# Kernel tuning notes

Hardware: AMD Instinct MI355X
Metric: run time of the kernel (lower is better)

## Reference

```python
import jax, jax.numpy as jnp
import numpy as np

DIM = 1536
NH = 12
HD = DIM // NH  # 128
B = 1
F, H, W = 8, 16, 16
S = F * H * W  # 2048
EPS = 1e-6
MAX_POS = 1024


def _rmsnorm(x, g):
    # WanRMSNorm: x * rsqrt(mean(x^2, -1) + eps) * weight  (computed in fp32)
    return x * jax.lax.rsqrt(jnp.mean(x * x, axis=-1, keepdims=True) + EPS) * g


def _rope_apply(x, grid_sizes, freqs):
    # x: [B, S, NH, HD]; freqs: [1024, HD//2] angles. Full (level-0) freqs_i path.
    f, h, w = [int(v) for v in np.asarray(grid_sizes[0])]
    c = HD // 2  # 64
    s0 = c - 2 * (c // 3)  # 22 (frame freqs)
    s1 = c // 3            # 21 (height / width freqs)
    p0 = freqs[:f, :s0]
    p1 = freqs[:h, s0:s0 + s1]
    p2 = freqs[:w, s0 + s1:]
    ang = jnp.concatenate([
        jnp.broadcast_to(p0[:, None, None, :], (f, h, w, s0)),
        jnp.broadcast_to(p1[None, :, None, :], (f, h, w, s1)),
        jnp.broadcast_to(p2[None, None, :, :], (f, h, w, s1)),
    ], axis=-1).reshape(f * h * w, 1, c)  # [S, 1, c]
    cos, sin = jnp.cos(ang), jnp.sin(ang)
    xr = x[0].reshape(S, NH, c, 2)  # pairs -> complex rotation
    x0, x1 = xr[..., 0], xr[..., 1]
    out = jnp.stack([x0 * cos - x1 * sin, x0 * sin + x1 * cos], axis=-1)
    return out.reshape(S, NH, HD)[None].astype(jnp.float32)  # [1, S, NH, HD]


def setup_inputs() -> dict:
    key = jax.random.key(0)
    ks = jax.random.split(key, 8)
    sc = 0.02
    return {
        "x": jax.random.normal(ks[0], (B, S, DIM), jnp.float32),
        "freqs": jax.random.uniform(ks[1], (MAX_POS, HD // 2), jnp.float32, 0.0, 2.0 * np.pi),
        "wq": jax.random.normal(ks[2], (DIM, DIM), jnp.float32) * sc,
        "bq": jnp.zeros((DIM,), jnp.float32),
        "wk": jax.random.normal(ks[3], (DIM, DIM), jnp.float32) * sc,
        "bk": jnp.zeros((DIM,), jnp.float32),
        "wv": jax.random.normal(ks[4], (DIM, DIM), jnp.float32) * sc,
        "bv": jnp.zeros((DIM,), jnp.float32),
        "wo": jax.random.normal(ks[5], (DIM, DIM), jnp.float32) * sc,
        "bo": jnp.zeros((DIM,), jnp.float32),
        "gq": jnp.ones((DIM,), jnp.float32),
        "gk": jnp.ones((DIM,), jnp.float32),
        "seq_lens": jnp.array([S], jnp.int32),
        "grid_sizes": jnp.array([[F, H, W]], jnp.int32),
    }


def reference(x, freqs, wq, bq, wk, bk, wv, bv, wo, bo, gq, gk, seq_lens, grid_sizes):
    b, s = x.shape[:2]
    q = _rmsnorm(x @ wq.T + bq, gq).reshape(b, s, NH, HD)
    k = _rmsnorm(x @ wk.T + bk, gk).reshape(b, s, NH, HD)
    v = (x @ wv.T + bv).reshape(b, s, NH, HD)
    q = _rope_apply(q, grid_sizes, freqs)
    k = _rope_apply(k, grid_sizes, freqs)
    # flash_attention with k_lens=seq_lens, full window -> masked SDPA
    kmask = jnp.arange(s)[None, :] < seq_lens[:, None]  # [b, s]
    scores = jnp.einsum('bqnd,bknd->bnqk', q, k) / np.sqrt(HD).astype(np.float32)
    scores = jnp.where(kmask[:, None, None, :], scores, jnp.finfo(scores.dtype).min)
    attn = jax.nn.softmax(scores, axis=-1)
    out = jnp.einsum('bnqk,bknd->bqnd', attn, v).reshape(b, s, DIM)
    return out @ wo.T + bo
```

## Files before the change

kernel.cpp:

```cpp
#include <hip/hip_runtime.h>
#include <math.h>

#define DIMN 1536
#define NHEAD 12
#define HDIM 128
#define SLEN 2048
#define EPSV 1e-6f

typedef __attribute__((ext_vector_type(8))) short short8;
typedef __attribute__((ext_vector_type(4))) short short4v;
typedef __attribute__((ext_vector_type(4))) float f32x4;

typedef __attribute__((address_space(1))) const void gvoid_t;
typedef __attribute__((address_space(3))) void lvoid_t;

__device__ __forceinline__ void gload_lds16(const void* g, void* l) {
    __builtin_amdgcn_global_load_lds((gvoid_t*)g, (lvoid_t*)l, 16, 0, 0);
}

__device__ inline short to_bf16(float f) {
    union { float f; unsigned u; } v; v.f = f;
    unsigned r = (v.u + 0x7FFFu + ((v.u >> 16) & 1u)) >> 16;
    return (short)r;
}
__device__ inline float bf_to_f(short h) {
    union { unsigned u; float f; } v;
    v.u = ((unsigned)(unsigned short)h) << 16;
    return v.f;
}

__device__ __forceinline__ int swz8(int row, int c) {
    return c ^ (row & 7);
}

__global__ __launch_bounds__(256)
void cast5(const float* s0, const float* s1, const float* s2,
           const float* s3, const float* s4,
           short* d0, short* d1, short* d2, short* d3, short* d4,
           int n0, int nw)
{
    const float* s; short* d; int n;
    switch (blockIdx.y) {
        case 0: s = s0; d = d0; n = n0; break;
        case 1: s = s1; d = d1; n = nw; break;
        case 2: s = s2; d = d2; n = nw; break;
        case 3: s = s3; d = d3; n = nw; break;
        default: s = s4; d = d4; n = nw; break;
    }
    int idx = (blockIdx.x * 256 + threadIdx.x) * 8;
    if (idx >= n) return;
    float4 a = *(const float4*)(s + idx);
    float4 b = *(const float4*)(s + idx + 4);
    short8 r;
    r[0] = to_bf16(a.x); r[1] = to_bf16(a.y); r[2] = to_bf16(a.z); r[3] = to_bf16(a.w);
    r[4] = to_bf16(b.x); r[5] = to_bf16(b.y); r[6] = to_bf16(b.z); r[7] = to_bf16(b.w);
    *(short8*)(d + idx) = r;
}

__device__ __forceinline__ void gemm_mainloop(const short* __restrict__ A,
    const short* __restrict__ W, int m0, int n0, int K,
    short* As, short* Bs, f32x4 (&acc)[4][4])
{
    const int tid = threadIdx.x;
    const int wave = tid >> 6, lane = tid & 63;
    const int quad = lane >> 4, col = lane & 15;
    const int wm = wave >> 1, wn = wave & 1;
    const int sr = tid >> 3;
    const int sc = tid & 7;

    for (int kt = 0; kt < K; kt += 64) {
        __syncthreads();
        #pragma unroll
        for (int i = 0; i < 4; ++i) {
            const int row = i * 32 + sr;
            const int c = swz8(row, sc);
            gload_lds16(A + (size_t)(m0 + row) * K + kt + c * 8, As + i * 2048 + tid * 8);
        }
        #pragma unroll
        for (int i = 0; i < 4; ++i) {
            const int row = i * 32 + sr;
            const int c = swz8(row, sc);
            gload_lds16(W + (size_t)(n0 + row) * K + kt + c * 8, Bs + i * 2048 + tid * 8);
        }
        __syncthreads();

        #pragma unroll
        for (int kb = 0; kb < 2; ++kb) {
            short8 af[4], bf[4];
            #pragma unroll
            for (int mt = 0; mt < 4; ++mt) {
                const int row = wm * 64 + mt * 16 + col;
                af[mt] = *(const short8*)&As[row * 64 + swz8(row, kb * 4 + quad) * 8];
            }
            #pragma unroll
            for (int nt = 0; nt < 4; ++nt) {
                const int row = wn * 64 + nt * 16 + col;
                bf[nt] = *(const short8*)&Bs[row * 64 + swz8(row, kb * 4 + quad) * 8];
            }
            #pragma unroll
            for (int mt = 0; mt < 4; ++mt)
                #pragma unroll
                for (int nt = 0; nt < 4; ++nt)
                    acc[mt][nt] = __builtin_amdgcn_mfma_f32_16x16x32_bf16(
                        af[mt], bf[nt], acc[mt][nt], 0, 0, 0);
        }
    }
}

__global__ __launch_bounds__(256)
void gemm_qkv(const short* __restrict__ A,
              const short* __restrict__ W0, const short* __restrict__ W1,
              const short* __restrict__ W2,
              const float* __restrict__ b0, const float* __restrict__ b1,
              const float* __restrict__ b2,
              short* __restrict__ Y0, short* __restrict__ Y1,
              short* __restrict__ Vp)
{
    __shared__ __attribute__((aligned(16))) short As[128 * 64];
    __shared__ __attribute__((aligned(16))) short Bs[128 * 64];

    const int sel = blockIdx.x / (DIMN / 128);
    const int nb  = blockIdx.x % (DIMN / 128);
    const short* W    = (sel == 0) ? W0 : (sel == 1) ? W1 : W2;
    const float* bias = (sel == 0) ? b0 : (sel == 1) ? b1 : b2;

    const int tid = threadIdx.x;
    const int wave = tid >> 6, lane = tid & 63;
    const int quad = lane >> 4, col = lane & 15;
    const int wm = wave >> 1, wn = wave & 1;
    const int m0 = blockIdx.y * 128, n0 = nb * 128;

    f32x4 acc[4][4];
    #pragma unroll
    for (int i = 0; i < 4; ++i)
        #pragma unroll
        for (int j = 0; j < 4; ++j)
            #pragma unroll
            for (int r = 0; r < 4; ++r) acc[i][j][r] = 0.f;

    gemm_mainloop(A, W, m0, n0, DIMN, As, Bs, acc);

    if (sel < 2) {
        short* Y = (sel == 0) ? Y0 : Y1;
        #pragma unroll
        for (int mt = 0; mt < 4; ++mt) {
            #pragma unroll
            for (int nt = 0; nt < 4; ++nt) {
                const int n = n0 + wn * 64 + nt * 16 + col;
                const float bb = bias[n];
                #pragma unroll
                for (int r = 0; r < 4; ++r) {
                    const int m = m0 + wm * 64 + mt * 16 + quad * 4 + r;
                    Y[(size_t)m * DIMN + n] = to_bf16(acc[mt][nt][r] + bb);
                }
            }
        }
    } else {
        const int head = nb;
        const int kt64 = blockIdx.y * 2 + wm;
        #pragma unroll
        for (int mt = 0; mt < 4; ++mt) {
            #pragma unroll
            for (int nt = 0; nt < 4; ++nt) {
                const int n = n0 + wn * 64 + nt * 16 + col;
                const float bb = bias[n];
                const int dt = wn * 4 + nt;
                const int chunk = (head * 64 + kt64 * 2 + (mt >> 1)) * 8 + dt;
                const int off = ((mt & 1) * 2 + (quad >> 1)) * 128 + col * 8 + (quad & 1) * 4;
                short4v o;
                #pragma unroll
                for (int r = 0; r < 4; ++r) o[r] = to_bf16(acc[mt][nt][r] + bb);
                *(short4v*)(Vp + (size_t)chunk * 512 + off) = o;
            }
        }
    }
}

__global__ __launch_bounds__(256)
void gemm_out(const short* __restrict__ A, const short* __restrict__ W,
              const float* __restrict__ bias, float* __restrict__ Yf)
{
    __shared__ __attribute__((aligned(16))) short As[128 * 64];
    __shared__ __attribute__((aligned(16))) short Bs[128 * 64];

    const int tid = threadIdx.x;
    const int wave = tid >> 6, lane = tid & 63;
    const int quad = lane >> 4, col = lane & 15;
    const int wm = wave >> 1, wn = wave & 1;
    const int m0 = blockIdx.y * 128, n0 = blockIdx.x * 128;

    f32x4 acc[4][4];
    #pragma unroll
    for (int i = 0; i < 4; ++i)
        #pragma unroll
        for (int j = 0; j < 4; ++j)
            #pragma unroll
            for (int r = 0; r < 4; ++r) acc[i][j][r] = 0.f;

    gemm_mainloop(A, W, m0, n0, DIMN, As, Bs, acc);

    #pragma unroll
    for (int mt = 0; mt < 4; ++mt) {
        #pragma unroll
        for (int nt = 0; nt < 4; ++nt) {
            const int n = n0 + wn * 64 + nt * 16 + col;
            const float bb = bias[n];
            #pragma unroll
            for (int r = 0; r < 4; ++r) {
                const int m = m0 + wm * 64 + mt * 16 + quad * 4 + r;
                Yf[(size_t)m * DIMN + n] = acc[mt][nt][r] + bb;
            }
        }
    }
}

__global__ __launch_bounds__(256)
void rms_rope_qk(short* __restrict__ qbuf, const short* __restrict__ kbuf,
                 short* __restrict__ Kp,
                 const float* __restrict__ gq, const float* __restrict__ gk,
                 const float* __restrict__ freqs, const int* __restrict__ grid_sizes)
{
    const int s = blockIdx.x;
    const int isK = blockIdx.y;
    const int tid = threadIdx.x;
    short* qrow = qbuf + (size_t)s * DIMN;
    const short* row = isK ? (kbuf + (size_t)s * DIMN) : qrow;
    const float* g = isK ? gk : gq;

    float ss = 0.f;
    if (tid < 192) {
        short8 v = *(const short8*)(row + tid * 8);
        #pragma unroll
        for (int j = 0; j < 8; ++j) { float f = bf_to_f(v[j]); ss += f * f; }
    }
    #pragma unroll
    for (int off = 32; off; off >>= 1) ss += __shfl_down(ss, off, 64);

    __shared__ float red[4];
    __shared__ float s_scale;
    if ((tid & 63) == 0) red[tid >> 6] = ss;
    __syncthreads();
    if (tid == 0) {
        float t = red[0] + red[1] + red[2] + red[3];
        float sc = rsqrtf(t / (float)DIMN + EPSV);
        s_scale = isK ? sc : sc * 0.08838834764831845f;
    }
    __syncthreads();
    const float scale = s_scale;

    const int h = grid_sizes[1], w = grid_sizes[2];
    const int fi = s / (h * w);
    const int hi = (s / w) % h;
    const int wi = s % w;

    if (!isK) {
        for (int p = tid; p < NHEAD * 64; p += 256) {
            const int n = p >> 6;
            const int d = p & 63;
            const int idx = (d < 22) ? fi : ((d < 43) ? hi : wi);
            const float ang = freqs[idx * 64 + d];
            float sn, cs;
            __sincosf(ang, &sn, &cs);
            const int base = n * HDIM + 2 * d;
            const float v0 = bf_to_f(qrow[base]) * scale * g[base];
            const float v1 = bf_to_f(qrow[base + 1]) * scale * g[base + 1];
            qrow[base]     = to_bf16(v0 * cs - v1 * sn);
            qrow[base + 1] = to_bf16(v0 * sn + v1 * cs);
        }
    } else if (tid < 192) {
        const int n = tid >> 4;
        const int o = tid & 15;
        short8 outv;
        #pragma unroll
        for (int pp = 0; pp < 4; ++pp) {
            const int pd = o * 4 + pp;
            const int idx = (pd < 22) ? fi : ((pd < 43) ? hi : wi);
            const float ang = freqs[idx * 64 + pd];
            float sn, cs;
            __sincosf(ang, &sn, &cs);
            const int base = n * HDIM + 2 * pd;
            const float v0 = bf_to_f(row[base]) * scale * g[base];
            const float v1 = bf_to_f(row[base + 1]) * scale * g[base + 1];
            outv[pp * 2]     = to_bf16(v0 * cs - v1 * sn);
            outv[pp * 2 + 1] = to_bf16(v0 * sn + v1 * cs);
        }
        const int kb = s >> 4, colk = s & 15;
        const int kc = o >> 2, quadk = o & 3;
        const size_t addr = ((((size_t)(n * 128 + kb) * 4 + kc) * 64) + quadk * 16 + colk) * 8;
        *(short8*)(Kp + addr) = outv;
    }
}

__global__ __launch_bounds__(128)
void attn_mfma11(const short* __restrict__ Q, const short* __restrict__ Kp,
                 const short* __restrict__ Vp, short* __restrict__ O,
                 const int* __restrict__ seq_lens)
{
    __shared__ __attribute__((aligned(16))) short psw[2 * 1280];
    __shared__ __attribute__((aligned(16))) float sacc[32 * 132];
    __shared__ float sl[32];

    const int tid  = threadIdx.x;
    const int wave = tid >> 6;
    const int lane = tid & 63;
    const int quad = lane >> 4, col = lane & 15;

    const int orig = blockIdx.y * 64 + blockIdx.x;
    const int work = (orig & 7) * 96 + (orig >> 3);
    const int head = work >> 6;
    const int row0 = (work & 63) * 32;
    const int slen = seq_lens[0];

    short8 qf[2][4];
    #pragma unroll
    for (int T = 0; T < 2; ++T)
        #pragma unroll
        for (int kc = 0; kc < 4; ++kc)
            qf[T][kc] = *(const short8*)(Q + (size_t)(row0 + T * 16 + col) * DIMN
                                         + head * HDIM + kc * 32 + quad * 8);

    f32x4 oacc[2][8];
    #pragma unroll
    for (int T = 0; T < 2; ++T)
        #pragma unroll
        for (int dt = 0; dt < 8; ++dt)
            #pragma unroll
            for (int r = 0; r < 4; ++r) oacc[T][dt][r] = 0.f;
    float lsum[2][4];
    #pragma unroll
    for (int T = 0; T < 2; ++T)
        #pragma unroll
        for (int r = 0; r < 4; ++r) lsum[T][r] = 0.f;

    const short* kbase = Kp + (size_t)head * 262144 + lane * 8;
    const short* vbase = Vp + (size_t)head * 262144 + lane * 8;
    short* pswm = psw + wave * 1280;
    const int step0 = wave * 32;

    auto loadKV = [&](short8 (&kf)[8], short8 (&vf)[8], int step) {
        const short* ks = kbase + (size_t)step * 4096;
        const short* vs = vbase + (size_t)step * 4096;
        #pragma unroll
        for (int c = 0; c < 8; ++c) kf[c] = *(const short8*)(ks + c * 512);
        #pragma unroll
        for (int c = 0; c < 8; ++c) vf[c] = *(const short8*)(vs + c * 512);
    };

    auto compute = [&](short8 (&kf)[8], short8 (&vf)[8], int step) {
        f32x4 s[2][2];
        #pragma unroll
        for (int T = 0; T < 2; ++T)
            #pragma unroll
            for (int nt = 0; nt < 2; ++nt)
                #pragma unroll
                for (int r = 0; r < 4; ++r) s[T][nt][r] = 0.f;

        #pragma unroll
        for (int kc = 0; kc < 4; ++kc)
            #pragma unroll
            for (int T = 0; T < 2; ++T) {
                s[T][0] = __builtin_amdgcn_mfma_f32_16x16x32_bf16(qf[T][kc], kf[kc],     s[T][0], 0, 0, 0);
                s[T][1] = __builtin_amdgcn_mfma_f32_16x16x32_bf16(qf[T][kc], kf[4 + kc], s[T][1], 0, 0, 0);
            }

        const int kt0 = step * 32;
        #pragma unroll
        for (int T = 0; T < 2; ++T)
            #pragma unroll
            for (int nt = 0; nt < 2; ++nt) {
                const bool masked = (kt0 + nt * 16 + col >= slen);
                #pragma unroll
                for (int r = 0; r < 4; ++r) {
                    float p = masked ? 0.f : __expf(s[T][nt][r]);
                    lsum[T][r] += p;
                    pswm[T * 640 + (quad * 4 + r) * 40 + nt * 16 + col] = to_bf16(p);
                }
            }

        short8 pf0 = *(const short8*)&pswm[col * 40 + quad * 8];
        short8 pf1 = *(const short8*)&pswm[640 + col * 40 + quad * 8];

        #pragma unroll
        for (int dt = 0; dt < 8; ++dt) {
            oacc[0][dt] = __builtin_amdgcn_mfma_f32_16x16x32_bf16(pf0, vf[dt], oacc[0][dt], 0, 0, 0);
            oacc[1][dt] = __builtin_amdgcn_mfma_f32_16x16x32_bf16(pf1, vf[dt], oacc[1][dt], 0, 0, 0);
        }
    };

    short8 kA[8], vA[8], kB[8], vB[8];
    loadKV(kA, vA, step0);

    #pragma unroll 1
    for (int kt = 0; kt < 32; kt += 2) {
        loadKV(kB, vB, step0 + kt + 1);
        compute(kA, vA, step0 + kt);
        loadKV(kA, vA, step0 + kt + 2);
        compute(kB, vB, step0 + kt + 1);
    }

    #pragma unroll
    for (int T = 0; T < 2; ++T)
        #pragma unroll
        for (int r = 0; r < 4; ++r) {
            #pragma unroll
            for (int off = 8; off; off >>= 1)
                lsum[T][r] += __shfl_xor(lsum[T][r], off, 64);
        }

    if (wave == 1) {
        #pragma unroll
        for (int T = 0; T < 2; ++T) {
            #pragma unroll
            for (int dt = 0; dt < 8; ++dt)
                #pragma unroll
                for (int r = 0; r < 4; ++r)
                    sacc[(T * 16 + quad * 4 + r) * 132 + dt * 16 + col] = oacc[T][dt][r];
            if (col == 0) {
                #pragma unroll
                for (int r = 0; r < 4; ++r) sl[T * 16 + quad * 4 + r] = lsum[T][r];
            }
        }
    }
    __syncthreads();
    if (wave == 0) {
        #pragma unroll
        for (int T = 0; T < 2; ++T) {
            float inv[4];
            #pragma unroll
            for (int r = 0; r < 4; ++r)
                inv[r] = 1.0f / (lsum[T][r] + sl[T * 16 + quad * 4 + r]);
            #pragma unroll
            for (int dt = 0; dt < 8; ++dt)
                #pragma unroll
                for (int r = 0; r < 4; ++r) {
                    const float o = oacc[T][dt][r]
                                  + sacc[(T * 16 + quad * 4 + r) * 132 + dt * 16 + col];
                    O[(size_t)(row0 + T * 16 + quad * 4 + r) * DIMN
                      + head * HDIM + dt * 16 + col] = to_bf16(o * inv[r]);
                }
        }
    }
}

extern "C" void kernel_launch(void* const* d_in, const int* in_sizes, int n_in,
                              void* d_out, int out_size, void* d_ws, size_t ws_size,
                              hipStream_t stream)
{
    const float* x     = (const float*)d_in[0];
    const float* freqs = (const float*)d_in[1];
    const float* wq    = (const float*)d_in[2];
    const float* bq    = (const float*)d_in[3];
    const float* wk    = (const float*)d_in[4];
    const float* bk    = (const float*)d_in[5];
    const float* wv    = (const float*)d_in[6];
    const float* bv    = (const float*)d_in[7];
    const float* wo    = (const float*)d_in[8];
    const float* bo    = (const float*)d_in[9];
    const float* gq    = (const float*)d_in[10];
    const float* gk    = (const float*)d_in[11];
    const int* seq_lens   = (const int*)d_in[12];
    const int* grid_sizes = (const int*)d_in[13];
    float* out = (float*)d_out;

    const size_t NX = (size_t)SLEN * DIMN;
    const size_t NW = (size_t)DIMN * DIMN;
    short* xb  = (short*)d_ws;
    short* wqb = xb + NX;
    short* wkb = wqb + NW;
    short* wvb = wkb + NW;
    short* wob = wvb + NW;
    short* qb  = wob + NW;
    short* kb  = qb + NX;
    short* vp  = kb + NX;
    short* kp  = vp + NX;
    short* ob  = kp + NX;

    cast5<<<dim3(1536, 5), 256, 0, stream>>>(x, wq, wk, wv, wo,
                                             xb, wqb, wkb, wvb, wob,
                                             (int)NX, (int)NW);

    gemm_qkv<<<dim3(3 * DIMN / 128, SLEN / 128), 256, 0, stream>>>(
        xb, wqb, wkb, wvb, bq, bk, bv, qb, kb, vp);

    rms_rope_qk<<<dim3(SLEN, 2), 256, 0, stream>>>(qb, kb, kp, gq, gk, freqs, grid_sizes);

    attn_mfma11<<<dim3(64, NHEAD), 128, 0, stream>>>(qb, kp, vp, ob, seq_lens);

    gemm_out<<<dim3(DIMN / 128, SLEN / 128), 256, 0, stream>>>(ob, wob, bo, out);
}
```

Measured before the change: 260.3 us.

## Double-buffer LDS tiles in GEMM mainloop to overlap loads with MFMA

Restructures the shared GEMM mainloop used by the QKV and output projections into a two-stage LDS ping-pong. The next K-tile is issued with global_load_lds into the alternate buffer before the MFMA work on the current buffer, and a single barrier per iteration replaces the two barriers it had before. The goal is to hide global-to-LDS load latency behind matrix compute. In exchange, LDS per block doubles to 64 KB, which lowers how many blocks can be resident per CU.

```diff
diff --git a/kernel.cpp b/kernel.cpp
--- a/kernel.cpp
+++ b/kernel.cpp
@@ -67,35 +67,40 @@
     const int wm = wave >> 1, wn = wave & 1;
     const int sr = tid >> 3;
     const int sc = tid & 7;
-
-    for (int kt = 0; kt < K; kt += 64) {
-        __syncthreads();
+    const int nk = K >> 6;
+
+    auto stage = [&](int buf, int kt) {
         #pragma unroll
         for (int i = 0; i < 4; ++i) {
             const int row = i * 32 + sr;
             const int c = swz8(row, sc);
-            gload_lds16(A + (size_t)(m0 + row) * K + kt + c * 8, As + i * 2048 + tid * 8);
+            gload_lds16(A + (size_t)(m0 + row) * K + kt * 64 + c * 8,
+                        As + buf * 8192 + i * 2048 + tid * 8);
         }
         #pragma unroll
         for (int i = 0; i < 4; ++i) {
             const int row = i * 32 + sr;
             const int c = swz8(row, sc);
-            gload_lds16(W + (size_t)(n0 + row) * K + kt + c * 8, Bs + i * 2048 + tid * 8);
-        }
-        __syncthreads();
-
+            gload_lds16(W + (size_t)(n0 + row) * K + kt * 64 + c * 8,
+                        Bs + buf * 8192 + i * 2048 + tid * 8);
+        }
+    };
+
+    auto compute = [&](int buf) {
+        const short* Ab = As + buf * 8192;
+        const short* Bb = Bs + buf * 8192;
         #pragma unroll
         for (int kb = 0; kb < 2; ++kb) {
             short8 af[4], bf[4];
             #pragma unroll
             for (int mt = 0; mt < 4; ++mt) {
                 const int row = wm * 64 + mt * 16 + col;
-                af[mt] = *(const short8*)&As[row * 64 + swz8(row, kb * 4 + quad) * 8];
+                af[mt] = *(const short8*)&Ab[row * 64 + swz8(row, kb * 4 + quad) * 8];
             }
             #pragma unroll
             for (int nt = 0; nt < 4; ++nt) {
                 const int row = wn * 64 + nt * 16 + col;
-                bf[nt] = *(const short8*)&Bs[row * 64 + swz8(row, kb * 4 + quad) * 8];
+                bf[nt] = *(const short8*)&Bb[row * 64 + swz8(row, kb * 4 + quad) * 8];
             }
             #pragma unroll
             for (int mt = 0; mt < 4; ++mt)
@@ -104,7 +109,19 @@
                     acc[mt][nt] = __builtin_amdgcn_mfma_f32_16x16x32_bf16(
                         af[mt], bf[nt], acc[mt][nt], 0, 0, 0);
         }
-    }
+    };
+
+    stage(0, 0);
+    __syncthreads();
+    int buf = 0;
+    #pragma unroll 1
+    for (int kt = 0; kt < nk - 1; ++kt) {
+        stage(buf ^ 1, kt + 1);
+        compute(buf);
+        __syncthreads();
+        buf ^= 1;
+    }
+    compute(buf);
 }
 
 __global__ __launch_bounds__(256)
@@ -116,8 +133,8 @@
               short* __restrict__ Y0, short* __restrict__ Y1,
               short* __restrict__ Vp)
 {
-    __shared__ __attribute__((aligned(16))) short As[128 * 64];
-    __shared__ __attribute__((aligned(16))) short Bs[128 * 64];
+    __shared__ __attribute__((aligned(16))) short As[2 * 128 * 64];
+    __shared__ __attribute__((aligned(16))) short Bs[2 * 128 * 64];
 
     const int sel = blockIdx.x / (DIMN / 128);
     const int nb  = blockIdx.x % (DIMN / 128);
@@ -180,8 +197,8 @@
 void gemm_out(const short* __restrict__ A, const short* __restrict__ W,
               const float* __restrict__ bias, float* __restrict__ Yf)
 {
-    __shared__ __attribute__((aligned(16))) short As[128 * 64];
-    __shared__ __attribute__((aligned(16))) short Bs[128 * 64];
+    __shared__ __attribute__((aligned(16))) short As[2 * 128 * 64];
+    __shared__ __attribute__((aligned(16))) short Bs[2 * 128 * 64];
 
     const int tid = threadIdx.x;
     const int wave = tid >> 6, lane = tid & 63;
```

Result: slower. 272.1 us (+4.5%).
